# Optimization experiments

Measured on AMD Instinct MI355X. Metric: run time of the kernel, lower is better.

Reference implementation:

```python
import jax, jax.numpy as jnp
import numpy as np

EMB, DK, DV = 768, 256, 256
B, N = 8, 2048


def setup_inputs() -> dict:
    key = jax.random.key(0)
    ks = jax.random.split(key, 9)
    s = 1.0 / np.sqrt(EMB)
    # Stack the 3 per-head Linear layers into [3, EMB, D] weights (same math).
    Wq = jax.random.uniform(ks[0], (3, EMB, DK), jnp.float32, -s, s)
    bq = jax.random.uniform(ks[1], (3, DK), jnp.float32, -s, s)
    Wk = jax.random.uniform(ks[2], (3, EMB, DK), jnp.float32, -s, s)
    bk = jax.random.uniform(ks[3], (3, DK), jnp.float32, -s, s)
    Wv = jax.random.uniform(ks[4], (3, EMB, DV), jnp.float32, -s, s)
    bv = jax.random.uniform(ks[5], (3, DV), jnp.float32, -s, s)
    s0 = 1.0 / np.sqrt(3 * DV)
    W0 = jax.random.uniform(ks[6], (3 * DV, EMB), jnp.float32, -s0, s0)
    b0 = jax.random.uniform(ks[7], (EMB,), jnp.float32, -s0, s0)
    x = jax.random.normal(ks[8], (B, N, EMB), jnp.float32)
    return {"x": x, "Wq": Wq, "bq": bq, "Wk": Wk, "bk": bk,
            "Wv": Wv, "bv": bv, "W0": W0, "b0": b0}


def reference(x, Wq, bq, Wk, bk, Wv, bv, W0, b0):
    # QKV for all 3 heads in one batched GEMM each: [B,3,N,D]
    Q = jnp.einsum('bne,hed->bhnd', x, Wq) + bq[None, :, None, :]
    K = jnp.einsum('bne,hed->bhnd', x, Wk) + bk[None, :, None, :]
    V = jnp.einsum('bne,hed->bhnd', x, Wv) + bv[None, :, None, :]
    scores = jnp.einsum('bhnd,bhmd->bhnm', Q, K) / jnp.sqrt(jnp.float32(DK))
    attn = jax.nn.softmax(scores, axis=-1)
    res = jnp.einsum('bhnm,bhmd->bhnd', attn, V)  # [B,3,N,DV]
    # concat heads along feature dim (head order matches torch concat order)
    res = jnp.transpose(res, (0, 2, 1, 3)).reshape(B, N, 3 * DV)
    return res @ W0 + b0
```

## Files before the change

### kernel.cpp

```cpp
#include <hip/hip_runtime.h>
#include <stdint.h>

typedef __attribute__((ext_vector_type(8))) short short8;
typedef __attribute__((ext_vector_type(4))) float floatx4;

#define EMB 768
#define DKV 256
#define NB  8
#define NS  2048

__device__ __forceinline__ float b2f(unsigned short u) {
  union { unsigned int i; float f; } v; v.i = ((unsigned int)u) << 16; return v.f;
}
__device__ __forceinline__ unsigned short f2b(float f) {
  union { float f; unsigned int i; } v; v.f = f;
  return (unsigned short)((v.i + 0x7FFFu + ((v.i >> 16) & 1u)) >> 16);
}

__device__ __forceinline__ short8 load8x(const void* p, size_t e, int f32) {
  short8 r;
  if (f32) {
    const float* f = (const float*)p + e;
    float4 a = *(const float4*)f;
    float4 b = *(const float4*)(f + 4);
    r[0] = (short)f2b(a.x); r[1] = (short)f2b(a.y);
    r[2] = (short)f2b(a.z); r[3] = (short)f2b(a.w);
    r[4] = (short)f2b(b.x); r[5] = (short)f2b(b.y);
    r[6] = (short)f2b(b.z); r[7] = (short)f2b(b.w);
  } else {
    r = *(const short8*)((const unsigned short*)p + e);
  }
  return r;
}
__device__ __forceinline__ float loadf(const void* p, size_t e, int f32) {
  return f32 ? ((const float*)p)[e] : b2f(((const unsigned short*)p)[e]);
}

__global__ __launch_bounds__(256) void detect_kernel(
    const unsigned short* __restrict__ x, int* __restrict__ flag) {
  __shared__ int cnt;
  if (threadIdx.x == 0) cnt = 0;
  __syncthreads();
  int bad = 0;
  for (int i = threadIdx.x; i < 1024; i += 256) {
    float v = b2f(x[i]);
    if (!(fabsf(v) <= 1e4f)) bad++;
  }
  atomicAdd(&cnt, bad);
  __syncthreads();
  if (threadIdx.x == 0) {
    flag[0] = (cnt > 16) ? 1 : 0;
    flag[1] = 0;
  }
}

__global__ __launch_bounds__(256) void repack_all(
    const void* __restrict__ Wq, const void* __restrict__ Wk,
    const void* __restrict__ Wv, const void* __restrict__ W0,
    const void* __restrict__ X,
    unsigned short* __restrict__ WT, unsigned short* __restrict__ W0T,
    unsigned short* __restrict__ Xb,
    const int* __restrict__ flag, int do_x) {
  __shared__ unsigned short tile[32][33];
  const int f32 = *flag;
  const int tid = threadIdx.x;
  const int b = blockIdx.x;

  if (b < 1728) {
    const int slab = b / 192;
    const int rem = b - slab * 192;
    const int k0 = (rem % 24) * 32, d0 = (rem / 24) * 32;
    const int t = slab / 3, h = slab - t * 3;
    const void* Wsrc = (t == 0) ? Wq : ((t == 1) ? Wk : Wv);
#pragma unroll
    for (int rr = 0; rr < 4; ++rr) {
      int ki = rr * 8 + (tid >> 5), di = tid & 31;
      tile[ki][di] = f2b(loadf(Wsrc, (size_t)(h * EMB + k0 + ki) * DKV + d0 + di, f32));
    }
    __syncthreads();
#pragma unroll
    for (int rr = 0; rr < 4; ++rr) {
      int di = rr * 8 + (tid >> 5), ki = tid & 31;
      WT[(size_t)(slab * 256 + d0 + di) * EMB + k0 + ki] = tile[ki][di];
    }
  } else if (b < 2304) {
    const int bb = b - 1728;
    const int k0 = (bb % 24) * 32, o0 = (bb / 24) * 32;
#pragma unroll
    for (int rr = 0; rr < 4; ++rr) {
      int ki = rr * 8 + (tid >> 5), oi = tid & 31;
      tile[ki][oi] = f2b(loadf(W0, (size_t)(k0 + ki) * EMB + o0 + oi, f32));
    }
    __syncthreads();
#pragma unroll
    for (int rr = 0; rr < 4; ++rr) {
      int oi = rr * 8 + (tid >> 5), ki = tid & 31;
      W0T[(size_t)(o0 + oi) * EMB + k0 + ki] = tile[ki][oi];
    }
  } else {
    if (!do_x) return;
    const int bb = b - 2304;
#pragma unroll
    for (int i = 0; i < 4; ++i) {
      size_t e = ((size_t)bb * 1024 + i * 256 + tid) * 8;
      short8 v = load8x(X, e, f32);
      *(short8*)&Xb[e] = v;
    }
  }
}

__global__ __launch_bounds__(256, 2) void kv_gemm(
    const void* __restrict__ Xs, const unsigned short* __restrict__ WT,
    const void* __restrict__ bk, const void* __restrict__ bv,
    unsigned short* __restrict__ Kb, unsigned short* __restrict__ Vtb,
    const int* __restrict__ xflag, const int* __restrict__ dflag) {
  __shared__ __align__(16) unsigned short As[128 * 40];
  __shared__ __align__(16) unsigned short BsK[128 * 40];
  __shared__ __align__(16) unsigned short BsV[128 * 40];
  const int xf32 = *xflag;
  const int f32 = *dflag;
  const int tid = threadIdx.x;
  const int wave = tid >> 6, lane = tid & 63, quad = lane >> 4, l15 = lane & 15;
  const int wm = wave >> 1, wn = wave & 1;
  const int row0 = blockIdx.y * 128;
  const int cb = blockIdx.x * 128;

  floatx4 accK[4][4], accV[4][4];
  for (int m = 0; m < 4; ++m)
    for (int n = 0; n < 4; ++n) { accK[m][n] = (floatx4)0.0f; accV[m][n] = (floatx4)0.0f; }

  const size_t arow0 = (size_t)row0 * EMB;
  const unsigned short* BbK = WT + (size_t)(768 + cb) * EMB;
  const unsigned short* BbV = WT + (size_t)(1536 + cb) * EMB;

  short8 va[2], vk[2], vv[2];
#pragma unroll
  for (int i = 0; i < 2; ++i) {
    int idx = i * 256 + tid;
    int r = idx >> 2, kp = (idx & 3) << 3;
    va[i] = load8x(Xs, arow0 + (size_t)r * EMB + kp, xf32);
    vk[i] = *(const short8*)(BbK + (size_t)r * EMB + kp);
    vv[i] = *(const short8*)(BbV + (size_t)r * EMB + kp);
  }

  for (int k0 = 0; k0 < EMB; k0 += 32) {
    __syncthreads();
#pragma unroll
    for (int i = 0; i < 2; ++i) {
      int idx = i * 256 + tid;
      int off = (idx >> 2) * 40 + (idx & 3) * 8;
      *(short8*)&As[off] = va[i];
      *(short8*)&BsK[off] = vk[i];
      *(short8*)&BsV[off] = vv[i];
    }
    if (k0 + 32 < EMB) {
      const int kn = k0 + 32;
#pragma unroll
      for (int i = 0; i < 2; ++i) {
        int idx = i * 256 + tid;
        int r = idx >> 2, kp = (idx & 3) << 3;
        va[i] = load8x(Xs, arow0 + (size_t)r * EMB + kn + kp, xf32);
        vk[i] = *(const short8*)(BbK + (size_t)r * EMB + kn + kp);
        vv[i] = *(const short8*)(BbV + (size_t)r * EMB + kn + kp);
      }
    }
    __syncthreads();
    short8 af[4], bk4[4], bv4[4];
#pragma unroll
    for (int m = 0; m < 4; ++m)
      af[m] = *(const short8*)&As[(wm * 64 + m * 16 + l15) * 40 + quad * 8];
#pragma unroll
    for (int n = 0; n < 4; ++n) {
      bk4[n] = *(const short8*)&BsK[(wn * 64 + n * 16 + l15) * 40 + quad * 8];
      bv4[n] = *(const short8*)&BsV[(wn * 64 + n * 16 + l15) * 40 + quad * 8];
    }
    __builtin_amdgcn_s_setprio(1);
#pragma unroll
    for (int n = 0; n < 4; ++n)
#pragma unroll
      for (int m = 0; m < 4; ++m) {
        accK[m][n] = __builtin_amdgcn_mfma_f32_16x16x32_bf16(af[m], bk4[n], accK[m][n], 0, 0, 0);
        accV[m][n] = __builtin_amdgcn_mfma_f32_16x16x32_bf16(af[m], bv4[n], accV[m][n], 0, 0, 0);
      }
    __builtin_amdgcn_s_setprio(0);
  }

  const int h = cb >> 8;
  const int dbase = cb & 255;

#pragma unroll
  for (int n = 0; n < 4; ++n) {
    const int cc = wn * 64 + n * 16 + l15;
    const float bvv = loadf(bk, h * 256 + dbase + cc, f32);
    const int d = dbase + cc;
#pragma unroll
    for (int m = 0; m < 4; ++m) {
      const int rbase = row0 + wm * 64 + m * 16 + quad * 4;
#pragma unroll
      for (int r = 0; r < 4; ++r) {
        const int row = rbase + r;
        const int bb = row >> 11, nn = row & 2047;
        Kb[((size_t)(bb * 3 + h) * 2048 + nn) * 256 + d] = f2b(accK[m][n][r] + bvv);
      }
    }
  }
#pragma unroll
  for (int n = 0; n < 4; ++n) {
    const int cc = wn * 64 + n * 16 + l15;
    const float bvv = loadf(bv, h * 256 + dbase + cc, f32);
    const int d = dbase + cc;
#pragma unroll
    for (int m = 0; m < 4; ++m) {
      const int rbase = row0 + wm * 64 + m * 16 + quad * 4;
      const int bb = rbase >> 11, nn = rbase & 2047;
      const size_t base = ((size_t)(bb * 3 + h) * 256 + d) * 2048 + nn;
      uint2 val;
      val.x = (uint32_t)f2b(accV[m][n][0] + bvv) | ((uint32_t)f2b(accV[m][n][1] + bvv) << 16);
      val.y = (uint32_t)f2b(accV[m][n][2] + bvv) | ((uint32_t)f2b(accV[m][n][3] + bvv) << 16);
      *(uint2*)(Vtb + base) = val;
    }
  }
}

__global__ __launch_bounds__(256, 3) void flash_fused(
    const void* __restrict__ Xs, const unsigned short* __restrict__ WT,
    const void* __restrict__ bq,
    const unsigned short* __restrict__ Kb, const unsigned short* __restrict__ Vtb,
    unsigned short* __restrict__ Ob,
    const int* __restrict__ xflag, const int* __restrict__ dflag) {
  __shared__ __align__(16) unsigned short smem[21248];
  unsigned short* AsQ = smem;
  unsigned short* BsQ = smem + 2560;
  unsigned short* Qs  = smem;
  unsigned short* Ks  = smem;
  unsigned short* Vts = smem + 8448;
  unsigned short* Ps  = smem + 18688;

  const int xf32 = *xflag;
  const int f32 = *dflag;
  const int tid = threadIdx.x;
  const int wave = tid >> 6, lane = tid & 63, quad = lane >> 4, l15 = lane & 15;
  const int bh = blockIdx.x;
  const int bb = bh / 3, hh = bh - bb * 3;
  const int q0 = blockIdx.y * 64;

  short8 qf[8];

  {
    const size_t xrow0 = (size_t)bb * NS + q0;
    floatx4 qacc[4][4];
    for (int m = 0; m < 4; ++m)
      for (int n = 0; n < 4; ++n) qacc[m][n] = (floatx4)0.0f;

    for (int k0 = 0; k0 < EMB; k0 += 32) {
      short8 va, vb[4];
      {
        int r = tid >> 2, kp = (tid & 3) << 3;
        va = load8x(Xs, (xrow0 + r) * EMB + k0 + kp, xf32);
      }
#pragma unroll
      for (int i = 0; i < 4; ++i) {
        int c = i * 256 + tid;
        int n = c >> 2, kp = (c & 3) << 3;
        vb[i] = *(const short8*)(WT + (size_t)(hh * 256 + n) * EMB + k0 + kp);
      }
      __syncthreads();
      *(short8*)&AsQ[(tid >> 2) * 40 + (tid & 3) * 8] = va;
#pragma unroll
      for (int i = 0; i < 4; ++i) {
        int c = i * 256 + tid;
        *(short8*)&BsQ[(c >> 2) * 40 + (c & 3) * 8] = vb[i];
      }
      __syncthreads();
      short8 af[4], bf[4];
#pragma unroll
      for (int m = 0; m < 4; ++m)
        af[m] = *(const short8*)&AsQ[(m * 16 + l15) * 40 + quad * 8];
#pragma unroll
      for (int n = 0; n < 4; ++n)
        bf[n] = *(const short8*)&BsQ[(wave * 64 + n * 16 + l15) * 40 + quad * 8];
      __builtin_amdgcn_s_setprio(1);
#pragma unroll
      for (int n = 0; n < 4; ++n)
#pragma unroll
        for (int m = 0; m < 4; ++m)
          qacc[m][n] = __builtin_amdgcn_mfma_f32_16x16x32_bf16(af[m], bf[n], qacc[m][n], 0, 0, 0);
      __builtin_amdgcn_s_setprio(0);
    }
    __syncthreads();

#pragma unroll
    for (int n = 0; n < 4; ++n) {
      const int col = wave * 64 + n * 16 + l15;
      const float bqv = loadf(bq, hh * 256 + col, f32);
#pragma unroll
      for (int m = 0; m < 4; ++m)
#pragma unroll
        for (int r = 0; r < 4; ++r)
          Qs[(m * 16 + quad * 4 + r) * 264 + col] = f2b((qacc[m][n][r] + bqv) * 0.0625f);
    }
    __syncthreads();
#pragma unroll
    for (int ks = 0; ks < 8; ++ks)
      qf[ks] = *(const short8*)&Qs[(wave * 16 + l15) * 264 + ks * 32 + quad * 8];
    __syncthreads();
  }

  const unsigned short* Kp = Kb + (size_t)bh * NS * DKV;
  const unsigned short* Vp = Vtb + (size_t)bh * DKV * NS;

  floatx4 oacc[4][4];
  for (int m = 0; m < 4; ++m)
    for (int ct = 0; ct < 4; ++ct) oacc[m][ct] = (floatx4)0.0f;
  float l_part = 0.f;

  for (int j0 = 0; j0 < NS; j0 += 32) {
    short8 kv[4], vv[4];
#pragma unroll
    for (int i = 0; i < 4; ++i) {
      int c = i * 256 + tid;
      kv[i] = *(const short8*)(Kp + (size_t)(j0 + (c >> 5)) * DKV + ((c & 31) << 3));
      vv[i] = *(const short8*)(Vp + (size_t)(c >> 2) * NS + j0 + ((c & 3) << 3));
    }
    __syncthreads();
#pragma unroll
    for (int i = 0; i < 4; ++i) {
      int c = i * 256 + tid;
      *(short8*)&Ks[(c >> 5) * 264 + (c & 31) * 8] = kv[i];
      *(short8*)&Vts[(c >> 2) * 40 + (c & 3) * 8] = vv[i];
    }
    __syncthreads();

    floatx4 sacc[2];
    sacc[0] = (floatx4)0.0f; sacc[1] = (floatx4)0.0f;
    __builtin_amdgcn_s_setprio(1);
#pragma unroll
    for (int ks = 0; ks < 8; ++ks)
#pragma unroll
      for (int ct = 0; ct < 2; ++ct) {
        short8 kfr = *(const short8*)&Ks[(ct * 16 + l15) * 264 + ks * 32 + quad * 8];
        sacc[ct] = __builtin_amdgcn_mfma_f32_16x16x32_bf16(kfr, qf[ks], sacc[ct], 0, 0, 0);
      }
    __builtin_amdgcn_s_setprio(0);

#pragma unroll
    for (int ct = 0; ct < 2; ++ct) {
      float p0 = __expf(sacc[ct][0]);
      float p1 = __expf(sacc[ct][1]);
      float p2 = __expf(sacc[ct][2]);
      float p3 = __expf(sacc[ct][3]);
      l_part += (p0 + p1) + (p2 + p3);
      uint2 pk;
      pk.x = (uint32_t)f2b(p0) | ((uint32_t)f2b(p1) << 16);
      pk.y = (uint32_t)f2b(p2) | ((uint32_t)f2b(p3) << 16);
      *(uint2*)&Ps[(wave * 16 + l15) * 40 + ct * 16 + quad * 4] = pk;
    }
    __syncthreads();

    short8 pa[4];
#pragma unroll
    for (int m = 0; m < 4; ++m)
      pa[m] = *(const short8*)&Ps[(m * 16 + l15) * 40 + quad * 8];
    __builtin_amdgcn_s_setprio(1);
#pragma unroll
    for (int ct = 0; ct < 4; ++ct) {
      short8 vb = *(const short8*)&Vts[(wave * 64 + ct * 16 + l15) * 40 + quad * 8];
#pragma unroll
      for (int m = 0; m < 4; ++m)
        oacc[m][ct] = __builtin_amdgcn_mfma_f32_16x16x32_bf16(pa[m], vb, oacc[m][ct], 0, 0, 0);
    }
    __builtin_amdgcn_s_setprio(0);
  }

  float l_r = l_part;
  l_r += __shfl_xor(l_r, 16);
  l_r += __shfl_xor(l_r, 32);

  __syncthreads();
  float* Lsf = (float*)smem;
  if (quad == 0) Lsf[wave * 16 + l15] = l_r;
  __syncthreads();

#pragma unroll
  for (int m = 0; m < 4; ++m) {
    float linv[4];
#pragma unroll
    for (int r = 0; r < 4; ++r) linv[r] = 1.0f / Lsf[m * 16 + quad * 4 + r];
#pragma unroll
    for (int ct = 0; ct < 4; ++ct) {
      const int col = hh * DKV + wave * 64 + ct * 16 + l15;
#pragma unroll
      for (int r = 0; r < 4; ++r) {
        const int n = q0 + m * 16 + quad * 4 + r;
        Ob[((size_t)(bb * NS + n)) * EMB + col] = f2b(oacc[m][ct][r] * linv[r]);
      }
    }
  }
}

__global__ __launch_bounds__(256) void out_gemm(
    const unsigned short* __restrict__ A, const unsigned short* __restrict__ W0T,
    const void* __restrict__ b0, void* __restrict__ out,
    const int* __restrict__ flag) {
  __shared__ __align__(16) unsigned short As[128 * 40];
  __shared__ __align__(16) unsigned short Bs[128 * 40];
  const int f32 = *flag;
  const int tid = threadIdx.x;
  const int wave = tid >> 6, lane = tid & 63, quad = lane >> 4, l15 = lane & 15;
  const int wm = wave >> 1, wn = wave & 1;
  const int row0 = blockIdx.y * 128;
  const int c0 = blockIdx.x * 128;

  floatx4 acc[4][4];
  for (int m = 0; m < 4; ++m)
    for (int n = 0; n < 4; ++n) acc[m][n] = (floatx4)0.0f;

  const unsigned short* Ab = A + (size_t)row0 * EMB;
  const unsigned short* Bb = W0T + (size_t)c0 * EMB;

  short8 va[2], vb[2];
#pragma unroll
  for (int i = 0; i < 2; ++i) {
    int idx = i * 256 + tid;
    int r = idx >> 2, kp = (idx & 3) << 3;
    va[i] = *(const short8*)(Ab + (size_t)r * EMB + kp);
    vb[i] = *(const short8*)(Bb + (size_t)r * EMB + kp);
  }

  for (int k0 = 0; k0 < EMB; k0 += 32) {
    __syncthreads();
#pragma unroll
    for (int i = 0; i < 2; ++i) {
      int idx = i * 256 + tid;
      *(short8*)&As[(idx >> 2) * 40 + (idx & 3) * 8] = va[i];
      *(short8*)&Bs[(idx >> 2) * 40 + (idx & 3) * 8] = vb[i];
    }
    if (k0 + 32 < EMB) {
      const int kn = k0 + 32;
#pragma unroll
      for (int i = 0; i < 2; ++i) {
        int idx = i * 256 + tid;
        int r = idx >> 2, kp = (idx & 3) << 3;
        va[i] = *(const short8*)(Ab + (size_t)r * EMB + kn + kp);
        vb[i] = *(const short8*)(Bb + (size_t)r * EMB + kn + kp);
      }
    }
    __syncthreads();
    short8 af[4], bf[4];
#pragma unroll
    for (int m = 0; m < 4; ++m)
      af[m] = *(const short8*)&As[(wm * 64 + m * 16 + l15) * 40 + quad * 8];
#pragma unroll
    for (int n = 0; n < 4; ++n)
      bf[n] = *(const short8*)&Bs[(wn * 64 + n * 16 + l15) * 40 + quad * 8];
    __builtin_amdgcn_s_setprio(1);
#pragma unroll
    for (int n = 0; n < 4; ++n)
#pragma unroll
      for (int m = 0; m < 4; ++m)
        acc[m][n] = __builtin_amdgcn_mfma_f32_16x16x32_bf16(af[m], bf[n], acc[m][n], 0, 0, 0);
    __builtin_amdgcn_s_setprio(0);
  }

#pragma unroll
  for (int n = 0; n < 4; ++n) {
    const int col = c0 + wn * 64 + n * 16 + l15;
    const float bvv = loadf(b0, col, f32);
#pragma unroll
    for (int m = 0; m < 4; ++m) {
      const int rbase = row0 + wm * 64 + m * 16 + quad * 4;
#pragma unroll
      for (int r = 0; r < 4; ++r) {
        const float v = acc[m][n][r] + bvv;
        const size_t idx = (size_t)(rbase + r) * EMB + col;
        if (f32) ((float*)out)[idx] = v;
        else     ((unsigned short*)out)[idx] = f2b(v);
      }
    }
  }
}

extern "C" void kernel_launch(void* const* d_in, const int* in_sizes, int n_in,
                              void* d_out, int out_size, void* d_ws, size_t ws_size,
                              hipStream_t stream) {
  const void* x  = d_in[0];
  const void* Wq = d_in[1];
  const void* bq = d_in[2];
  const void* Wk = d_in[3];
  const void* bk = d_in[4];
  const void* Wv = d_in[5];
  const void* bv = d_in[6];
  const void* W0 = d_in[7];
  const void* b0 = d_in[8];

  unsigned short* ws = (unsigned short*)d_ws;
  const size_t SZ = (size_t)NB * 3 * NS * DKV;
  unsigned short* Kb  = (unsigned short*)d_out;
  unsigned short* Vtb = ws;
  unsigned short* Ob  = ws + SZ;
  unsigned short* WT  = ws + 2 * SZ;
  unsigned short* W0T = WT + (size_t)2304 * EMB;
  int* flag = (int*)(W0T + (size_t)EMB * EMB);
  unsigned short* Xb = (unsigned short*)((char*)flag + 16);

  const size_t need = ((size_t)3 * SZ + (size_t)2304 * EMB + (size_t)EMB * EMB) * 2 + 16;
  const int use_xb = (ws_size >= need) ? 1 : 0;

  const void* x_gemm = use_xb ? (const void*)Xb : x;
  const int* xflag   = use_xb ? (flag + 1) : flag;

  detect_kernel<<<dim3(1), dim3(256), 0, stream>>>((const unsigned short*)x, flag);
  repack_all<<<dim3(3840), dim3(256), 0, stream>>>(Wq, Wk, Wv, W0, x, WT, W0T, Xb, flag, use_xb);
  kv_gemm<<<dim3(6, 128), dim3(256), 0, stream>>>(x_gemm, WT, bk, bv, Kb, Vtb, xflag, flag);
  flash_fused<<<dim3(24, 32), dim3(256), 0, stream>>>(x_gemm, WT, bq, Kb, Vtb, Ob, xflag, flag);
  out_gemm<<<dim3(6, 128), dim3(256), 0, stream>>>(Ob, W0T, b0, d_out, flag);
}
```

Baseline: 387.1 us.

## Use direct global-to-LDS loads with XOR-swizzled tiles in projection GEMMs

In the KV projection GEMM and the output projection GEMM, the register-staged software prefetch is replaced by `global_load_lds` instructions that write 16-byte chunks straight into shared memory. The padded LDS rows (stride 40) become unpadded 32-wide rows with an XOR swizzle on the 8-element chunk index, which is meant to avoid bank conflicts. The intent is to cut VGPR pressure and the extra register-to-LDS store instructions. The cost is that the next tile is no longer prefetched while the current one is computed, so each iteration waits on global latency before its barrier. The f32-input branch still goes through registers, using the same swizzled layout.

Result: slower. 396.8 us (+2.5%).

```diff
diff --git a/kernel.cpp b/kernel.cpp
--- a/kernel.cpp
+++ b/kernel.cpp
@@ -36,6 +36,12 @@
   return f32 ? ((const float*)p)[e] : b2f(((const unsigned short*)p)[e]);
 }
 
+__device__ __forceinline__ void gl_lds16(const void* g, void* l) {
+  __builtin_amdgcn_global_load_lds(
+      (const __attribute__((address_space(1))) void*)g,
+      (__attribute__((address_space(3))) void*)l, 16, 0, 0);
+}
+
 __global__ __launch_bounds__(256) void detect_kernel(
     const unsigned short* __restrict__ x, int* __restrict__ flag) {
   __shared__ int cnt;
@@ -114,9 +120,9 @@
     const void* __restrict__ bk, const void* __restrict__ bv,
     unsigned short* __restrict__ Kb, unsigned short* __restrict__ Vtb,
     const int* __restrict__ xflag, const int* __restrict__ dflag) {
-  __shared__ __align__(16) unsigned short As[128 * 40];
-  __shared__ __align__(16) unsigned short BsK[128 * 40];
-  __shared__ __align__(16) unsigned short BsV[128 * 40];
+  __shared__ __align__(16) unsigned short As[128 * 32];
+  __shared__ __align__(16) unsigned short BsK[128 * 32];
+  __shared__ __align__(16) unsigned short BsV[128 * 32];
   const int xf32 = *xflag;
   const int f32 = *dflag;
   const int tid = threadIdx.x;
@@ -129,50 +135,51 @@
   for (int m = 0; m < 4; ++m)
     for (int n = 0; n < 4; ++n) { accK[m][n] = (floatx4)0.0f; accV[m][n] = (floatx4)0.0f; }
 
-  const size_t arow0 = (size_t)row0 * EMB;
+  const unsigned short* Axb = (const unsigned short*)Xs;
   const unsigned short* BbK = WT + (size_t)(768 + cb) * EMB;
   const unsigned short* BbV = WT + (size_t)(1536 + cb) * EMB;
 
-  short8 va[2], vk[2], vv[2];
-#pragma unroll
-  for (int i = 0; i < 2; ++i) {
-    int idx = i * 256 + tid;
-    int r = idx >> 2, kp = (idx & 3) << 3;
-    va[i] = load8x(Xs, arow0 + (size_t)r * EMB + kp, xf32);
-    vk[i] = *(const short8*)(BbK + (size_t)r * EMB + kp);
-    vv[i] = *(const short8*)(BbV + (size_t)r * EMB + kp);
-  }
+  const int grow = (lane >> 2);
+  const int gch8 = (((lane & 3) ^ (grow & 3)) << 3);
 
   for (int k0 = 0; k0 < EMB; k0 += 32) {
     __syncthreads();
 #pragma unroll
     for (int i = 0; i < 2; ++i) {
-      int idx = i * 256 + tid;
-      int off = (idx >> 2) * 40 + (idx & 3) * 8;
-      *(short8*)&As[off] = va[i];
-      *(short8*)&BsK[off] = vk[i];
-      *(short8*)&BsV[off] = vv[i];
-    }
-    if (k0 + 32 < EMB) {
-      const int kn = k0 + 32;
+      const int j = wave * 2 + i;
+      const int row = j * 16 + grow;
+      gl_lds16(BbK + (size_t)row * EMB + k0 + gch8, &BsK[j * 512]);
+      gl_lds16(BbV + (size_t)row * EMB + k0 + gch8, &BsV[j * 512]);
+    }
+    if (!xf32) {
 #pragma unroll
       for (int i = 0; i < 2; ++i) {
-        int idx = i * 256 + tid;
-        int r = idx >> 2, kp = (idx & 3) << 3;
-        va[i] = load8x(Xs, arow0 + (size_t)r * EMB + kn + kp, xf32);
-        vk[i] = *(const short8*)(BbK + (size_t)r * EMB + kn + kp);
-        vv[i] = *(const short8*)(BbV + (size_t)r * EMB + kn + kp);
+        const int j = wave * 2 + i;
+        const int row = j * 16 + grow;
+        gl_lds16(Axb + (size_t)(row0 + row) * EMB + k0 + gch8, &As[j * 512]);
+      }
+    } else {
+#pragma unroll
+      for (int i = 0; i < 2; ++i) {
+        int cid = tid * 2 + i;
+        int row = cid >> 2, ch = cid & 3;
+        short8 v = load8x(Xs, (size_t)(row0 + row) * EMB + k0 + ((ch ^ (row & 3)) << 3), 1);
+        *(short8*)&As[row * 32 + ch * 8] = v;
       }
     }
     __syncthreads();
     short8 af[4], bk4[4], bv4[4];
 #pragma unroll
-    for (int m = 0; m < 4; ++m)
-      af[m] = *(const short8*)&As[(wm * 64 + m * 16 + l15) * 40 + quad * 8];
+    for (int m = 0; m < 4; ++m) {
+      const int row = wm * 64 + m * 16 + l15;
+      af[m] = *(const short8*)&As[row * 32 + ((quad ^ (l15 & 3)) << 3)];
+    }
 #pragma unroll
     for (int n = 0; n < 4; ++n) {
-      bk4[n] = *(const short8*)&BsK[(wn * 64 + n * 16 + l15) * 40 + quad * 8];
-      bv4[n] = *(const short8*)&BsV[(wn * 64 + n * 16 + l15) * 40 + quad * 8];
+      const int row = wn * 64 + n * 16 + l15;
+      const int off = row * 32 + ((quad ^ (l15 & 3)) << 3);
+      bk4[n] = *(const short8*)&BsK[off];
+      bv4[n] = *(const short8*)&BsV[off];
     }
     __builtin_amdgcn_s_setprio(1);
 #pragma unroll
@@ -402,8 +409,8 @@
     const unsigned short* __restrict__ A, const unsigned short* __restrict__ W0T,
     const void* __restrict__ b0, void* __restrict__ out,
     const int* __restrict__ flag) {
-  __shared__ __align__(16) unsigned short As[128 * 40];
-  __shared__ __align__(16) unsigned short Bs[128 * 40];
+  __shared__ __align__(16) unsigned short As[128 * 32];
+  __shared__ __align__(16) unsigned short Bs[128 * 32];
   const int f32 = *flag;
   const int tid = threadIdx.x;
   const int wave = tid >> 6, lane = tid & 63, quad = lane >> 4, l15 = lane & 15;
@@ -418,41 +425,30 @@
   const unsigned short* Ab = A + (size_t)row0 * EMB;
   const unsigned short* Bb = W0T + (size_t)c0 * EMB;
 
-  short8 va[2], vb[2];
-#pragma unroll
-  for (int i = 0; i < 2; ++i) {
-    int idx = i * 256 + tid;
-    int r = idx >> 2, kp = (idx & 3) << 3;
-    va[i] = *(const short8*)(Ab + (size_t)r * EMB + kp);
-    vb[i] = *(const short8*)(Bb + (size_t)r * EMB + kp);
-  }
+  const int grow = (lane >> 2);
+  const int gch8 = (((lane & 3) ^ (grow & 3)) << 3);
 
   for (int k0 = 0; k0 < EMB; k0 += 32) {
     __syncthreads();
 #pragma unroll
     for (int i = 0; i < 2; ++i) {
-      int idx = i * 256 + tid;
-      *(short8*)&As[(idx >> 2) * 40 + (idx & 3) * 8] = va[i];
-      *(short8*)&Bs[(idx >> 2) * 40 + (idx & 3) * 8] = vb[i];
-    }
-    if (k0 + 32 < EMB) {
-      const int kn = k0 + 32;
-#pragma unroll
-      for (int i = 0; i < 2; ++i) {
-        int idx = i * 256 + tid;
-        int r = idx >> 2, kp = (idx & 3) << 3;
-        va[i] = *(const short8*)(Ab + (size_t)r * EMB + kn + kp);
-        vb[i] = *(const short8*)(Bb + (size_t)r * EMB + kn + kp);
-      }
+      const int j = wave * 2 + i;
+      const int row = j * 16 + grow;
+      gl_lds16(Ab + (size_t)row * EMB + k0 + gch8, &As[j * 512]);
+      gl_lds16(Bb + (size_t)row * EMB + k0 + gch8, &Bs[j * 512]);
     }
     __syncthreads();
     short8 af[4], bf[4];
 #pragma unroll
-    for (int m = 0; m < 4; ++m)
-      af[m] = *(const short8*)&As[(wm * 64 + m * 16 + l15) * 40 + quad * 8];
-#pragma unroll
-    for (int n = 0; n < 4; ++n)
-      bf[n] = *(const short8*)&Bs[(wn * 64 + n * 16 + l15) * 40 + quad * 8];
+    for (int m = 0; m < 4; ++m) {
+      const int row = wm * 64 + m * 16 + l15;
+      af[m] = *(const short8*)&As[row * 32 + ((quad ^ (l15 & 3)) << 3)];
+    }
+#pragma unroll
+    for (int n = 0; n < 4; ++n) {
+      const int row = wn * 64 + n * 16 + l15;
+      bf[n] = *(const short8*)&Bs[row * 32 + ((quad ^ (l15 & 3)) << 3)];
+    }
     __builtin_amdgcn_s_setprio(1);
 #pragma unroll
     for (int n = 0; n < 4; ++n)
```

## Load K/V tiles directly into LDS with XOR-swizzled layout

Applied to the files above, without the earlier changes.

Replaces the register-staged global-to-LDS copy of K and V tiles in the flash attention loop with direct global_load_lds 16-byte transfers. The padded LDS rows are dropped in favour of XOR-swizzled column groups to avoid bank conflicts on the MFMA fragment reads, which also shrinks shared memory use. The goal is to cut VGPR pressure and the extra LDS write instructions. The trade-off is that the loads are still synchronous per iteration, and the swizzle must match between the writers and the readers.

Measured after the change: 374.8 us. 1.03x faster.

```diff
diff --git a/kernel.cpp b/kernel.cpp
--- a/kernel.cpp
+++ b/kernel.cpp
@@ -34,6 +34,12 @@
 }
 __device__ __forceinline__ float loadf(const void* p, size_t e, int f32) {
   return f32 ? ((const float*)p)[e] : b2f(((const unsigned short*)p)[e]);
+}
+
+__device__ __forceinline__ void gl_lds16(const void* g, void* l) {
+  __builtin_amdgcn_global_load_lds(
+      (const __attribute__((address_space(1))) void*)g,
+      (__attribute__((address_space(3))) void*)l, 16, 0, 0);
 }
 
 __global__ __launch_bounds__(256) void detect_kernel(
@@ -228,13 +234,13 @@
     const unsigned short* __restrict__ Kb, const unsigned short* __restrict__ Vtb,
     unsigned short* __restrict__ Ob,
     const int* __restrict__ xflag, const int* __restrict__ dflag) {
-  __shared__ __align__(16) unsigned short smem[21248];
+  __shared__ __align__(16) unsigned short smem[18944];
   unsigned short* AsQ = smem;
   unsigned short* BsQ = smem + 2560;
   unsigned short* Qs  = smem;
   unsigned short* Ks  = smem;
-  unsigned short* Vts = smem + 8448;
-  unsigned short* Ps  = smem + 18688;
+  unsigned short* Vts = smem + 8192;
+  unsigned short* Ps  = smem + 16384;
 
   const int xf32 = *xflag;
   const int f32 = *dflag;
@@ -314,20 +320,22 @@
     for (int ct = 0; ct < 4; ++ct) oacc[m][ct] = (floatx4)0.0f;
   float l_part = 0.f;
 
+  const int krow_in = lane >> 5;
+  const int kc16 = lane & 31;
+  const int vrow_in = lane >> 2;
+  const int vc = lane & 3;
+
   for (int j0 = 0; j0 < NS; j0 += 32) {
-    short8 kv[4], vv[4];
+    __syncthreads();
 #pragma unroll
     for (int i = 0; i < 4; ++i) {
-      int c = i * 256 + tid;
-      kv[i] = *(const short8*)(Kp + (size_t)(j0 + (c >> 5)) * DKV + ((c & 31) << 3));
-      vv[i] = *(const short8*)(Vp + (size_t)(c >> 2) * NS + j0 + ((c & 3) << 3));
-    }
-    __syncthreads();
-#pragma unroll
-    for (int i = 0; i < 4; ++i) {
-      int c = i * 256 + tid;
-      *(short8*)&Ks[(c >> 5) * 264 + (c & 31) * 8] = kv[i];
-      *(short8*)&Vts[(c >> 2) * 40 + (c & 3) * 8] = vv[i];
+      const int L = wave * 4 + i;
+      const int krow = L * 2 + krow_in;
+      const int kg = kc16 ^ (krow & 7);
+      gl_lds16(Kp + (size_t)(j0 + krow) * DKV + kg * 8, &Ks[L * 512]);
+      const int vd = L * 16 + vrow_in;
+      const int vg = vc ^ ((vd >> 1) & 3);
+      gl_lds16(Vp + (size_t)vd * NS + j0 + vg * 8, &Vts[L * 512]);
     }
     __syncthreads();
 
@@ -338,7 +346,8 @@
     for (int ks = 0; ks < 8; ++ks)
 #pragma unroll
       for (int ct = 0; ct < 2; ++ct) {
-        short8 kfr = *(const short8*)&Ks[(ct * 16 + l15) * 264 + ks * 32 + quad * 8];
+        short8 kfr = *(const short8*)&Ks[(ct * 16 + l15) * 256 +
+                                         (((ks * 4 + quad) ^ (l15 & 7)) << 3)];
         sacc[ct] = __builtin_amdgcn_mfma_f32_16x16x32_bf16(kfr, qf[ks], sacc[ct], 0, 0, 0);
       }
     __builtin_amdgcn_s_setprio(0);
@@ -364,7 +373,8 @@
     __builtin_amdgcn_s_setprio(1);
 #pragma unroll
     for (int ct = 0; ct < 4; ++ct) {
-      short8 vb = *(const short8*)&Vts[(wave * 64 + ct * 16 + l15) * 40 + quad * 8];
+      const int rv = wave * 64 + ct * 16 + l15;
+      short8 vb = *(const short8*)&Vts[rv * 32 + ((quad ^ ((rv >> 1) & 3)) << 3)];
 #pragma unroll
       for (int m = 0; m < 4; ++m)
         oacc[m][ct] = __builtin_amdgcn_mfma_f32_16x16x32_bf16(pa[m], vb, oacc[m][ct], 0, 0, 0);
```
